# Optimization experiments

Measured on AMD Instinct MI355X. Metric: run time of the kernel, lower is better.

## Reference

```python
import jax, jax.numpy as jnp
import numpy as np

BLOCK = 32  # GGML quantization block size (Q4_0 style)
Q_OFFSET = 8.0  # 4-bit values stored unsigned in [0,16), centered by -8


def setup_inputs() -> dict:
    key = jax.random.key(0)
    k1, k2, k3, k4, k5, k6 = jax.random.split(key, 6)
    O, I, R, T = 4096, 4096, 16, 8192
    x = jax.random.normal(k1, (T, I), dtype=jnp.float32)
    qweight = jax.random.randint(k2, (O, I), 0, 16, dtype=jnp.int32)
    scales = jax.random.uniform(k3, (O, I // BLOCK), dtype=jnp.float32)
    lora_a = jax.random.normal(k4, (O, R), dtype=jnp.float32)
    lora_b = jax.random.normal(k5, (R, I), dtype=jnp.float32)
    bias = jax.random.normal(k6, (O,), dtype=jnp.float32)
    return {"x": x, "qweight": qweight, "scales": scales,
            "lora_a": lora_a, "lora_b": lora_b, "bias": bias}


def reference(x, qweight, scales, lora_a, lora_b, bias):
    # --- dequantize_tensor: per-block scale * centered int codes ---
    O, I = qweight.shape
    q = qweight.astype(jnp.float32) - Q_OFFSET            # [O, I]
    w = (q.reshape(O, I // BLOCK, BLOCK) * scales[:, :, None]).reshape(O, I)
    # --- patch application (LoRA-style additive patch) ---
    w = w + lora_a @ lora_b                               # [O, I]
    # --- downstream consumption: linear layer ---
    y = x @ w.T + bias                                    # [T, O]
    return y
```

## Files before the change

### kernel.cpp

```cpp
#include <hip/hip_runtime.h>
#include <hip/hip_bf16.h>

typedef unsigned short u16;
typedef __attribute__((ext_vector_type(4))) float f32x4;
typedef __attribute__((ext_vector_type(8))) short bf16x8;
typedef __attribute__((ext_vector_type(8))) u16 u16x8;

#define GLDS16(g, l) __builtin_amdgcn_global_load_lds( \
    (const __attribute__((address_space(1))) void*)(g), \
    (__attribute__((address_space(3))) void*)(l), 16, 0, 0)

__device__ inline u16 f2bf(float f) {
  union { float f; unsigned u; } v; v.f = f;
  unsigned r = v.u + 0x7fffu + ((v.u >> 16) & 1u);
  return (u16)(r >> 16);
}

__global__ __launch_bounds__(256) void k_dequant_lora(
    const int* __restrict__ qw, const float* __restrict__ sc,
    const float* __restrict__ la, const float* __restrict__ lb,
    u16* __restrict__ W)
{
  const int I = 4096, R = 16;
  __shared__ float lbs[16][512];
  __shared__ float las[256];
  const int c0 = blockIdx.x * 512;
  const int o0 = blockIdx.y * 16;
  const int tid = threadIdx.x;

  las[tid] = la[(size_t)(o0 + (tid >> 4)) * R + (tid & 15)];
  #pragma unroll
  for (int i = 0; i < 8; ++i) {
    int idx = tid + i * 256;
    int r = idx >> 7;
    int cc4 = (idx & 127) << 2;
    *(float4*)&lbs[r][cc4] = *(const float4*)&lb[(size_t)r * I + c0 + cc4];
  }
  __syncthreads();

  const int cc = (tid & 63) * 8;
  const int rg = tid >> 6;
  #pragma unroll
  for (int rr = 0; rr < 4; ++rr) {
    const int o = o0 + rg * 4 + rr;
    float acc[8] = {0.f,0.f,0.f,0.f,0.f,0.f,0.f,0.f};
    #pragma unroll
    for (int r = 0; r < 16; ++r) {
      float av = las[(rg * 4 + rr) * 16 + r];
      float4 b0 = *(const float4*)&lbs[r][cc];
      float4 b1 = *(const float4*)&lbs[r][cc + 4];
      acc[0] += av * b0.x; acc[1] += av * b0.y;
      acc[2] += av * b0.z; acc[3] += av * b0.w;
      acc[4] += av * b1.x; acc[5] += av * b1.y;
      acc[6] += av * b1.z; acc[7] += av * b1.w;
    }
    const int4* qp = (const int4*)&qw[(size_t)o * I + c0 + cc];
    int4 q0 = qp[0], q1 = qp[1];
    float s = sc[(size_t)o * (I / 32) + ((c0 + cc) >> 5)];
    u16x8 w;
    w[0] = f2bf(((float)q0.x - 8.0f) * s + acc[0]);
    w[1] = f2bf(((float)q0.y - 8.0f) * s + acc[1]);
    w[2] = f2bf(((float)q0.z - 8.0f) * s + acc[2]);
    w[3] = f2bf(((float)q0.w - 8.0f) * s + acc[3]);
    w[4] = f2bf(((float)q1.x - 8.0f) * s + acc[4]);
    w[5] = f2bf(((float)q1.y - 8.0f) * s + acc[5]);
    w[6] = f2bf(((float)q1.z - 8.0f) * s + acc[6]);
    w[7] = f2bf(((float)q1.w - 8.0f) * s + acc[7]);
    *(u16x8*)&W[(size_t)o * I + c0 + cc] = w;
  }
}

__global__ __launch_bounds__(256) void k_cvt(const float* __restrict__ x,
                                             u16* __restrict__ xb)
{
  const size_t n = (size_t)8192 * 4096;
  const size_t stride = (size_t)gridDim.x * 256 * 8;
  for (size_t i = ((size_t)blockIdx.x * 256 + threadIdx.x) * 8; i < n; i += stride) {
    float4 a = *(const float4*)&x[i];
    float4 b = *(const float4*)&x[i + 4];
    u16x8 o;
    o[0] = f2bf(a.x); o[1] = f2bf(a.y); o[2] = f2bf(a.z); o[3] = f2bf(a.w);
    o[4] = f2bf(b.x); o[5] = f2bf(b.y); o[6] = f2bf(b.z); o[7] = f2bf(b.w);
    *(u16x8*)&xb[i] = o;
  }
}

__global__ __launch_bounds__(512, 1) void k_gemm(
    const u16* __restrict__ A, const u16* __restrict__ B,
    const float* __restrict__ bias, float* __restrict__ C)
{
  const int N = 4096, K = 4096;
  const int NTK = 128;
  __shared__ u16 As[4 * 8192];
  __shared__ u16 Bs[4 * 8192];

  const int bid = blockIdx.x;
  const int swz = (bid & 7) * 64 + (bid >> 3);
  const int m0 = (swz >> 4) * 256;
  const int n0 = (swz & 15) * 256;

  const int tid = threadIdx.x;
  const int wid = tid >> 6, lane = tid & 63;
  const int wid_m = wid >> 2, wid_n = wid & 3;

  const int st0 = wid;
  const int st1 = 8 + wid;
  const int srow = lane >> 2;
  const int schunk = (((lane & 3) ^ (((lane >> 5) & 1) << 1))) * 8;
  const u16* Asrc0 = A + (size_t)(m0 + st0 * 16 + srow) * K + schunk;
  const u16* Asrc1 = A + (size_t)(m0 + st1 * 16 + srow) * K + schunk;
  const u16* Bsrc0 = B + (size_t)(n0 + st0 * 16 + srow) * K + schunk;
  const u16* Bsrc1 = B + (size_t)(n0 + st1 * 16 + srow) * K + schunk;

#define STAGE_A(buf, t) do { \
    GLDS16(Asrc0 + (size_t)(t) * 32, &As[(buf) * 8192 + st0 * 512]); \
    GLDS16(Asrc1 + (size_t)(t) * 32, &As[(buf) * 8192 + st1 * 512]); } while (0)
#define STAGE_B(buf, t) do { \
    GLDS16(Bsrc0 + (size_t)(t) * 32, &Bs[(buf) * 8192 + st0 * 512]); \
    GLDS16(Bsrc1 + (size_t)(t) * 32, &Bs[(buf) * 8192 + st1 * 512]); } while (0)

  const int LA = (lane & 15) * 32 + (((lane >> 4) * 8) ^ ((lane & 8) ? 16 : 0));
  const int wmb = wid_m * 8;
  const int wnb = wid_n * 4;

  f32x4 acc[8][4] = {};
  bf16x8 af[4], bf[4];

  STAGE_A(0, 0); STAGE_B(0, 0);
  STAGE_A(1, 1); STAGE_B(1, 1);
  asm volatile("s_waitcnt vmcnt(4)" ::: "memory");
  __builtin_amdgcn_s_barrier();

  for (int t = 0; t < NTK; ++t) {
    const int b_ = t & 3;

    #pragma unroll
    for (int m = 0; m < 4; ++m)
      af[m] = *(const bf16x8*)&As[b_ * 8192 + (wmb + m) * 512 + LA];
    #pragma unroll
    for (int n = 0; n < 4; ++n)
      bf[n] = *(const bf16x8*)&Bs[b_ * 8192 + (wnb + n) * 512 + LA];
    if (t + 2 < NTK) STAGE_A((t + 2) & 3, t + 2);
    __builtin_amdgcn_sched_barrier(0);
    __builtin_amdgcn_s_barrier();
    asm volatile("s_waitcnt lgkmcnt(0)" ::: "memory");
    __builtin_amdgcn_sched_barrier(0);
    __builtin_amdgcn_s_setprio(1);
    #pragma unroll
    for (int m = 0; m < 4; ++m)
      #pragma unroll
      for (int n = 0; n < 4; ++n)
        acc[m][n] = __builtin_amdgcn_mfma_f32_16x16x32_bf16(af[m], bf[n], acc[m][n], 0, 0, 0);
    __builtin_amdgcn_s_setprio(0);
    __builtin_amdgcn_sched_barrier(0);
    __builtin_amdgcn_s_barrier();

    #pragma unroll
    for (int m = 0; m < 4; ++m)
      af[m] = *(const bf16x8*)&As[b_ * 8192 + (wmb + 4 + m) * 512 + LA];
    if (t + 2 < NTK) {
      STAGE_B((t + 2) & 3, t + 2);
      asm volatile("s_waitcnt vmcnt(4)" ::: "memory");
    } else {
      asm volatile("s_waitcnt vmcnt(0)" ::: "memory");
    }
    __builtin_amdgcn_sched_barrier(0);
    __builtin_amdgcn_s_barrier();
    asm volatile("s_waitcnt lgkmcnt(0)" ::: "memory");
    __builtin_amdgcn_sched_barrier(0);
    __builtin_amdgcn_s_setprio(1);
    #pragma unroll
    for (int m = 0; m < 4; ++m)
      #pragma unroll
      for (int n = 0; n < 4; ++n)
        acc[4 + m][n] = __builtin_amdgcn_mfma_f32_16x16x32_bf16(af[m], bf[n], acc[4 + m][n], 0, 0, 0);
    __builtin_amdgcn_s_setprio(0);
    __builtin_amdgcn_sched_barrier(0);
    __builtin_amdgcn_s_barrier();
  }
#undef STAGE_A
#undef STAGE_B

  const int crow = m0 + wid_m * 128 + ((lane >> 4) << 2);
  const int ccol = n0 + wid_n * 64 + (lane & 15);
  #pragma unroll
  for (int n = 0; n < 4; ++n) {
    float bv = bias[ccol + n * 16];
    #pragma unroll
    for (int m = 0; m < 8; ++m) {
      #pragma unroll
      for (int j = 0; j < 4; ++j) {
        C[(size_t)(crow + m * 16 + j) * N + ccol + n * 16] = acc[m][n][j] + bv;
      }
    }
  }
}

extern "C" void kernel_launch(void* const* d_in, const int* in_sizes, int n_in,
                              void* d_out, int out_size, void* d_ws, size_t ws_size,
                              hipStream_t stream) {
  const float* x    = (const float*)d_in[0];
  const int*   qw   = (const int*)d_in[1];
  const float* sc   = (const float*)d_in[2];
  const float* la   = (const float*)d_in[3];
  const float* lb   = (const float*)d_in[4];
  const float* bias = (const float*)d_in[5];
  float* y = (float*)d_out;

  u16* W  = (u16*)d_ws;
  u16* Xb = (u16*)((char*)d_ws + (size_t)32 * 1024 * 1024);

  dim3 gridD(4096 / 512, 4096 / 16);
  k_dequant_lora<<<gridD, 256, 0, stream>>>(qw, sc, la, lb, W);
  k_cvt<<<2048, 256, 0, stream>>>(x, Xb);
  const int ngemm = (8192 / 256) * (4096 / 256);
  k_gemm<<<ngemm, 512, 0, stream>>>(Xb, W, bias, y);
}
```

Baseline: 370.2 us.

## Fuse prep kernels and split GEMM K-step into four finer load/MFMA phases

The dequant+LoRA kernel and the x-to-bf16 conversion are merged into one 2048-block launch. Each block does one W tile and a fixed 16K-element chunk of x, which removes a kernel boundary and its tail. The GEMM inner loop now runs four phases per K-step instead of two. Each phase loads two A fragments, issues one global-to-LDS prefetch and runs 8 MFMAs, so fewer A fragment registers are live and the prefetches are spread out. In exchange the MFMA bursts are shorter between barriers, which may expose more sync overhead.

```diff
diff --git a/kernel.cpp b/kernel.cpp
--- a/kernel.cpp
+++ b/kernel.cpp
@@ -16,16 +16,18 @@
   return (u16)(r >> 16);
 }
 
-__global__ __launch_bounds__(256) void k_dequant_lora(
+__global__ __launch_bounds__(256) void k_prep(
     const int* __restrict__ qw, const float* __restrict__ sc,
     const float* __restrict__ la, const float* __restrict__ lb,
-    u16* __restrict__ W)
+    const float* __restrict__ x,
+    u16* __restrict__ W, u16* __restrict__ xb)
 {
   const int I = 4096, R = 16;
   __shared__ float lbs[16][512];
   __shared__ float las[256];
-  const int c0 = blockIdx.x * 512;
-  const int o0 = blockIdx.y * 16;
+  const int b = blockIdx.x;
+  const int c0 = (b & 7) * 512;
+  const int o0 = (b >> 3) * 16;
   const int tid = threadIdx.x;
 
   las[tid] = la[(size_t)(o0 + (tid >> 4)) * R + (tid & 15)];
@@ -68,19 +70,16 @@
     w[7] = f2bf(((float)q1.w - 8.0f) * s + acc[7]);
     *(u16x8*)&W[(size_t)o * I + c0 + cc] = w;
   }
-}
-
-__global__ __launch_bounds__(256) void k_cvt(const float* __restrict__ x,
-                                             u16* __restrict__ xb)
-{
-  const size_t n = (size_t)8192 * 4096;
-  const size_t stride = (size_t)gridDim.x * 256 * 8;
-  for (size_t i = ((size_t)blockIdx.x * 256 + threadIdx.x) * 8; i < n; i += stride) {
+
+  const size_t base = (size_t)b * 16384;
+  #pragma unroll
+  for (int it = 0; it < 8; ++it) {
+    size_t i = base + (size_t)it * 2048 + (size_t)tid * 8;
     float4 a = *(const float4*)&x[i];
-    float4 b = *(const float4*)&x[i + 4];
+    float4 c = *(const float4*)&x[i + 4];
     u16x8 o;
     o[0] = f2bf(a.x); o[1] = f2bf(a.y); o[2] = f2bf(a.z); o[3] = f2bf(a.w);
-    o[4] = f2bf(b.x); o[5] = f2bf(b.y); o[6] = f2bf(b.z); o[7] = f2bf(b.w);
+    o[4] = f2bf(c.x); o[5] = f2bf(c.y); o[6] = f2bf(c.z); o[7] = f2bf(c.w);
     *(u16x8*)&xb[i] = o;
   }
 }
@@ -112,54 +111,83 @@
   const u16* Bsrc0 = B + (size_t)(n0 + st0 * 16 + srow) * K + schunk;
   const u16* Bsrc1 = B + (size_t)(n0 + st1 * 16 + srow) * K + schunk;
 
-#define STAGE_A(buf, t) do { \
-    GLDS16(Asrc0 + (size_t)(t) * 32, &As[(buf) * 8192 + st0 * 512]); \
-    GLDS16(Asrc1 + (size_t)(t) * 32, &As[(buf) * 8192 + st1 * 512]); } while (0)
-#define STAGE_B(buf, t) do { \
-    GLDS16(Bsrc0 + (size_t)(t) * 32, &Bs[(buf) * 8192 + st0 * 512]); \
-    GLDS16(Bsrc1 + (size_t)(t) * 32, &Bs[(buf) * 8192 + st1 * 512]); } while (0)
-
   const int LA = (lane & 15) * 32 + (((lane >> 4) * 8) ^ ((lane & 8) ? 16 : 0));
   const int wmb = wid_m * 8;
   const int wnb = wid_n * 4;
 
   f32x4 acc[8][4] = {};
-  bf16x8 af[4], bf[4];
-
-  STAGE_A(0, 0); STAGE_B(0, 0);
-  STAGE_A(1, 1); STAGE_B(1, 1);
+
+  GLDS16(Asrc0, &As[st0 * 512]);
+  GLDS16(Asrc1, &As[st1 * 512]);
+  GLDS16(Bsrc0, &Bs[st0 * 512]);
+  GLDS16(Bsrc1, &Bs[st1 * 512]);
+  GLDS16(Asrc0 + 32, &As[8192 + st0 * 512]);
+  GLDS16(Asrc1 + 32, &As[8192 + st1 * 512]);
+  GLDS16(Bsrc0 + 32, &Bs[8192 + st0 * 512]);
+  GLDS16(Bsrc1 + 32, &Bs[8192 + st1 * 512]);
   asm volatile("s_waitcnt vmcnt(4)" ::: "memory");
   __builtin_amdgcn_s_barrier();
 
   for (int t = 0; t < NTK; ++t) {
     const int b_ = t & 3;
-
-    #pragma unroll
-    for (int m = 0; m < 4; ++m)
-      af[m] = *(const bf16x8*)&As[b_ * 8192 + (wmb + m) * 512 + LA];
+    const int bs_ = (t + 2) & 3;
+    const bool stg = (t + 2 < NTK);
+    const u16* Ab = &As[b_ * 8192];
+    const u16* Bb = &Bs[b_ * 8192];
+    bf16x8 bfr[4], a0, a1;
+
     #pragma unroll
     for (int n = 0; n < 4; ++n)
-      bf[n] = *(const bf16x8*)&Bs[b_ * 8192 + (wnb + n) * 512 + LA];
-    if (t + 2 < NTK) STAGE_A((t + 2) & 3, t + 2);
-    __builtin_amdgcn_sched_barrier(0);
-    __builtin_amdgcn_s_barrier();
-    asm volatile("s_waitcnt lgkmcnt(0)" ::: "memory");
-    __builtin_amdgcn_sched_barrier(0);
-    __builtin_amdgcn_s_setprio(1);
-    #pragma unroll
-    for (int m = 0; m < 4; ++m)
-      #pragma unroll
-      for (int n = 0; n < 4; ++n)
-        acc[m][n] = __builtin_amdgcn_mfma_f32_16x16x32_bf16(af[m], bf[n], acc[m][n], 0, 0, 0);
-    __builtin_amdgcn_s_setprio(0);
-    __builtin_amdgcn_sched_barrier(0);
-    __builtin_amdgcn_s_barrier();
-
-    #pragma unroll
-    for (int m = 0; m < 4; ++m)
-      af[m] = *(const bf16x8*)&As[b_ * 8192 + (wmb + 4 + m) * 512 + LA];
-    if (t + 2 < NTK) {
-      STAGE_B((t + 2) & 3, t + 2);
+      bfr[n] = *(const bf16x8*)&Bb[(wnb + n) * 512 + LA];
+    a0 = *(const bf16x8*)&Ab[(wmb + 0) * 512 + LA];
+    a1 = *(const bf16x8*)&Ab[(wmb + 1) * 512 + LA];
+    if (stg) GLDS16(Asrc0 + (size_t)(t + 2) * 32, &As[bs_ * 8192 + st0 * 512]);
+    __builtin_amdgcn_sched_barrier(0);
+    __builtin_amdgcn_s_barrier();
+    asm volatile("s_waitcnt lgkmcnt(0)" ::: "memory");
+    __builtin_amdgcn_sched_barrier(0);
+    __builtin_amdgcn_s_setprio(1);
+    #pragma unroll
+    for (int n = 0; n < 4; ++n) {
+      acc[0][n] = __builtin_amdgcn_mfma_f32_16x16x32_bf16(a0, bfr[n], acc[0][n], 0, 0, 0);
+      acc[1][n] = __builtin_amdgcn_mfma_f32_16x16x32_bf16(a1, bfr[n], acc[1][n], 0, 0, 0);
+    }
+    __builtin_amdgcn_s_setprio(0);
+
+    a0 = *(const bf16x8*)&Ab[(wmb + 2) * 512 + LA];
+    a1 = *(const bf16x8*)&Ab[(wmb + 3) * 512 + LA];
+    if (stg) GLDS16(Asrc1 + (size_t)(t + 2) * 32, &As[bs_ * 8192 + st1 * 512]);
+    __builtin_amdgcn_sched_barrier(0);
+    __builtin_amdgcn_s_barrier();
+    asm volatile("s_waitcnt lgkmcnt(0)" ::: "memory");
+    __builtin_amdgcn_sched_barrier(0);
+    __builtin_amdgcn_s_setprio(1);
+    #pragma unroll
+    for (int n = 0; n < 4; ++n) {
+      acc[2][n] = __builtin_amdgcn_mfma_f32_16x16x32_bf16(a0, bfr[n], acc[2][n], 0, 0, 0);
+      acc[3][n] = __builtin_amdgcn_mfma_f32_16x16x32_bf16(a1, bfr[n], acc[3][n], 0, 0, 0);
+    }
+    __builtin_amdgcn_s_setprio(0);
+
+    a0 = *(const bf16x8*)&Ab[(wmb + 4) * 512 + LA];
+    a1 = *(const bf16x8*)&Ab[(wmb + 5) * 512 + LA];
+    if (stg) GLDS16(Bsrc0 + (size_t)(t + 2) * 32, &Bs[bs_ * 8192 + st0 * 512]);
+    __builtin_amdgcn_sched_barrier(0);
+    __builtin_amdgcn_s_barrier();
+    asm volatile("s_waitcnt lgkmcnt(0)" ::: "memory");
+    __builtin_amdgcn_sched_barrier(0);
+    __builtin_amdgcn_s_setprio(1);
+    #pragma unroll
+    for (int n = 0; n < 4; ++n) {
+      acc[4][n] = __builtin_amdgcn_mfma_f32_16x16x32_bf16(a0, bfr[n], acc[4][n], 0, 0, 0);
+      acc[5][n] = __builtin_amdgcn_mfma_f32_16x16x32_bf16(a1, bfr[n], acc[5][n], 0, 0, 0);
+    }
+    __builtin_amdgcn_s_setprio(0);
+
+    a0 = *(const bf16x8*)&Ab[(wmb + 6) * 512 + LA];
+    a1 = *(const bf16x8*)&Ab[(wmb + 7) * 512 + LA];
+    if (stg) {
+      GLDS16(Bsrc1 + (size_t)(t + 2) * 32, &Bs[bs_ * 8192 + st1 * 512]);
       asm volatile("s_waitcnt vmcnt(4)" ::: "memory");
     } else {
       asm volatile("s_waitcnt vmcnt(0)" ::: "memory");
@@ -170,16 +198,12 @@
     __builtin_amdgcn_sched_barrier(0);
     __builtin_amdgcn_s_setprio(1);
     #pragma unroll
-    for (int m = 0; m < 4; ++m)
-      #pragma unroll
-      for (int n = 0; n < 4; ++n)
-        acc[4 + m][n] = __builtin_amdgcn_mfma_f32_16x16x32_bf16(af[m], bf[n], acc[4 + m][n], 0, 0, 0);
-    __builtin_amdgcn_s_setprio(0);
-    __builtin_amdgcn_sched_barrier(0);
-    __builtin_amdgcn_s_barrier();
-  }
-#undef STAGE_A
-#undef STAGE_B
+    for (int n = 0; n < 4; ++n) {
+      acc[6][n] = __builtin_amdgcn_mfma_f32_16x16x32_bf16(a0, bfr[n], acc[6][n], 0, 0, 0);
+      acc[7][n] = __builtin_amdgcn_mfma_f32_16x16x32_bf16(a1, bfr[n], acc[7][n], 0, 0, 0);
+    }
+    __builtin_amdgcn_s_setprio(0);
+  }
 
   const int crow = m0 + wid_m * 128 + ((lane >> 4) << 2);
   const int ccol = n0 + wid_n * 64 + (lane & 15);
@@ -210,9 +234,7 @@
   u16* W  = (u16*)d_ws;
   u16* Xb = (u16*)((char*)d_ws + (size_t)32 * 1024 * 1024);
 
-  dim3 gridD(4096 / 512, 4096 / 16);
-  k_dequant_lora<<<gridD, 256, 0, stream>>>(qw, sc, la, lb, W);
-  k_cvt<<<2048, 256, 0, stream>>>(x, Xb);
+  k_prep<<<2048, 256, 0, stream>>>(qw, sc, la, lb, x, W, Xb);
   const int ngemm = (8192 / 256) * (4096 / 256);
   k_gemm<<<ngemm, 512, 0, stream>>>(Xb, W, bias, y);
 }
```

Result: slower. 421.7 us (+13.9%).
